# Kernel tuning notes

Measured on AMD Instinct MI355X. Metric: run time of the kernel, lower is better.

The kernel has to match this reference:

```python
import jax, jax.numpy as jnp
import numpy as np

C = 256
CQK = C // 8  # query/key channels


def setup_inputs() -> dict:
    key = jax.random.key(0)
    ks = jax.random.split(key, 7)
    B, H, W = 4, 64, 64
    x = jax.random.normal(ks[0], (B, C, H, W), dtype=jnp.float32)
    # 1x1 conv weights stored as [out_ch, in_ch] (kernel spatial dims are 1)
    sc = 1.0 / np.sqrt(C)
    Wq = jax.random.uniform(ks[1], (CQK, C), jnp.float32, -sc, sc)
    bq = jax.random.uniform(ks[2], (CQK,), jnp.float32, -sc, sc)
    Wk = jax.random.uniform(ks[3], (CQK, C), jnp.float32, -sc, sc)
    bk = jax.random.uniform(ks[4], (CQK,), jnp.float32, -sc, sc)
    Wv = jax.random.uniform(ks[5], (C, C), jnp.float32, -sc, sc)
    bv = jax.random.uniform(ks[6], (C,), jnp.float32, -sc, sc)
    gamma = jnp.zeros((1,), dtype=jnp.float32)
    return {"x": x, "Wq": Wq, "bq": bq, "Wk": Wk, "bk": bk, "Wv": Wv, "bv": bv, "gamma": gamma}


def reference(x, Wq, bq, Wk, bk, Wv, bv, gamma):
    B, Ch, H, W = x.shape
    N = H * W
    xf = x.reshape(B, Ch, N)  # [B, C, N]
    # 1x1 convs == per-pixel linear projections
    q = jnp.einsum('oc,bcn->bno', Wq, xf) + bq  # [B, N, CQK]
    k = jnp.einsum('oc,bcn->bon', Wk, xf) + bk[None, :, None]  # [B, CQK, N]
    v = jnp.einsum('oc,bcn->bon', Wv, xf) + bv[None, :, None]  # [B, C, N]
    s = jnp.einsum('bnd,bdm->bnm', q, k)  # [B, N, N]
    attn = jax.nn.softmax(s, axis=-1)
    # out[b,c,i] = sum_j v[b,c,j] * attn[b,i,j]
    out = jnp.einsum('bcj,bij->bci', v, attn).reshape(B, Ch, H, W)
    return x + gamma[0] * out
```

## Files before the change

kernel.cpp:

```cpp
#include <hip/hip_runtime.h>
#include <math.h>

#define BATCH 4
#define CCH   256
#define DQK   32
#define NPIX  4096
#define LOG2E 1.44269504088896340736f

typedef __attribute__((ext_vector_type(8)))  short          short8_t;
typedef __attribute__((ext_vector_type(4)))  unsigned short ushort4_t;
typedef __attribute__((ext_vector_type(8)))  unsigned short ushort8_t;
typedef __attribute__((ext_vector_type(16))) float          f32x16;
typedef __attribute__((ext_vector_type(2)))  unsigned int   uint2_t;

#if __has_builtin(__builtin_amdgcn_exp2f)
#define EXP2F(x) __builtin_amdgcn_exp2f(x)
#else
#define EXP2F(x) exp2f(x)
#endif

#define MFMA32(a, b, c) __builtin_amdgcn_mfma_f32_32x32x16_bf16(a, b, c, 0, 0, 0)

static __device__ __forceinline__ unsigned short f2bf(float f) {
    union { float f; unsigned int u; } v; v.f = f;
    unsigned int r = v.u + 0x7FFFu + ((v.u >> 16) & 1u);
    return (unsigned short)(r >> 16);
}

static __device__ __forceinline__ short8_t cat8(ushort4_t a, ushort4_t b) {
    ushort8_t c = __builtin_shufflevector(a, b, 0, 1, 2, 3, 4, 5, 6, 7);
    short8_t r; __builtin_memcpy(&r, &c, 16); return r;
}

static __device__ __forceinline__ short8_t u4_to_s8(const unsigned int* u) {
    short8_t r; __builtin_memcpy(&r, u, 16); return r;
}

static __device__ __forceinline__ uint2_t plswap(unsigned int a, unsigned int b) {
#if __has_builtin(__builtin_amdgcn_permlane32_swap)
    return __builtin_amdgcn_permlane32_swap(a, b, false, false);
#else
    const unsigned int sa = (unsigned int)__shfl_xor((int)a, 32);
    const unsigned int sb = (unsigned int)__shfl_xor((int)b, 32);
    const int h = (threadIdx.x >> 5) & 1;
    uint2_t r;
    r.x = h ? sb : a;
    r.y = h ? b : sa;
    return r;
#endif
}

static __device__ __forceinline__ void make_bfrag(
    const f32x16& s, float& l0, float& l1, unsigned int bfr[2][4])
{
    float pv[16];
    #pragma unroll
    for (int r = 0; r < 16; ++r) pv[r] = EXP2F(s[r]);
    #pragma unroll
    for (int r = 0; r < 16; r += 2) { l0 += pv[r]; l1 += pv[r + 1]; }
    unsigned int P[8];
    #pragma unroll
    for (int v = 0; v < 8; ++v)
        P[v] = __builtin_amdgcn_perm(__float_as_uint(pv[2 * v + 1]),
                                     __float_as_uint(pv[2 * v]), 0x07060302u);
    #pragma unroll
    for (int kp = 0; kp < 2; ++kp) {
        const uint2_t r02 = plswap(P[4 * kp + 0], P[4 * kp + 2]);
        const uint2_t r13 = plswap(P[4 * kp + 1], P[4 * kp + 3]);
        bfr[kp][0] = r02.x; bfr[kp][1] = r13.x;
        bfr[kp][2] = r02.y; bfr[kp][3] = r13.y;
    }
}

__global__ __launch_bounds__(256) void wconv_kernel(
    const float* __restrict__ Wq, const float* __restrict__ Wk,
    const float* __restrict__ Wv, unsigned short* __restrict__ wbf)
{
    const int idx = blockIdx.x * 256 + threadIdx.x;
    const int o = idx >> 8, c = idx & 255;
    float v;
    if (o < 32)      v = Wq[o * 256 + c] * LOG2E;
    else if (o < 64) v = Wk[(o - 32) * 256 + c];
    else             v = Wv[(o - 64) * 256 + c];
    wbf[((c >> 3) * 320 + o) * 8 + (c & 7)] = f2bf(v);
}

__global__ __launch_bounds__(256) void xt_kernel(
    const float* __restrict__ x, unsigned short* __restrict__ xfrag)
{
    const int b  = blockIdx.x >> 6;
    const int cg = (blockIdx.x >> 4) & 3;
    const int ng = blockIdx.x & 15;
    const int t  = threadIdx.x;
    const int w = t >> 6, l = t & 63;

    #pragma unroll
    for (int sgl = 0; sgl < 2; ++sgl) {
        const int sg = w * 2 + sgl;
        float f[4][8];
        #pragma unroll
        for (int p = 0; p < 8; ++p) {
            const float* row = x + ((size_t)(b * CCH + cg * 64 + sg * 8 + p)) * NPIX
                                 + ng * 256;
            #pragma unroll
            for (int j = 0; j < 4; ++j)
                f[j][p] = row[j * 64 + l];
        }
        #pragma unroll
        for (int j = 0; j < 4; ++j) {
            unsigned int d[4];
            #pragma unroll
            for (int k = 0; k < 4; ++k)
                d[k] = __builtin_amdgcn_perm(__float_as_uint(f[j][2 * k + 1]),
                                             __float_as_uint(f[j][2 * k]), 0x07060302u);
            const int nt = ng * 8 + j * 2 + (l >> 5);
            unsigned short* dst = xfrag +
                ((((size_t)(b * 128 + nt) * 32) + cg * 8 + sg) * 32 + (l & 31)) * 8;
            *(short8_t*)dst = u4_to_s8(d);
        }
    }
}

__global__ __launch_bounds__(320) void proj_kernel(
    const unsigned short* __restrict__ xfrag, const unsigned short* __restrict__ wbf,
    const float* __restrict__ bq, const float* __restrict__ bk,
    const float* __restrict__ bv,
    unsigned short* __restrict__ qfrag, unsigned short* __restrict__ kfrag,
    unsigned short* __restrict__ vfrag)
{
    __shared__ unsigned short qkb[2 * 2 * 32 * 40];
    __shared__ unsigned short vbuf[4 * 64 * 72];

    const int b   = blockIdx.x >> 6;
    const int nt0 = (blockIdx.x & 63) << 1;
    const int t   = threadIdx.x;
    const int w = t >> 6, lane = t & 63, il = lane & 31, h = lane >> 5;

    float4 bA[4], bB[4];
    #pragma unroll
    for (int g = 0; g < 4; ++g) {
        if (w == 0) {
            bA[g] = *(const float4*)&bq[8 * g + 4 * h];
            bB[g] = *(const float4*)&bk[8 * g + 4 * h];
        } else {
            bA[g] = *(const float4*)&bv[(w - 1) * 64 + 8 * g + 4 * h];
            bB[g] = *(const float4*)&bv[(w - 1) * 64 + 32 + 8 * g + 4 * h];
        }
    }

    f32x16 acc[2][2];
    #pragma unroll
    for (int a = 0; a < 2; ++a)
        #pragma unroll
        for (int i = 0; i < 2; ++i)
            #pragma unroll
            for (int r = 0; r < 16; ++r) acc[a][i][r] = 0.f;

    const unsigned short* wp = wbf + ((size_t)(h * 320 + w * 64 + il)) * 8;
    const unsigned short* xp0 = xfrag + (((size_t)(b * 128 + nt0) * 32 + h) * 32 + il) * 8;
    const unsigned short* xp1 = xp0 + (size_t)32 * 32 * 8;

    #pragma unroll 4
    for (int ks = 0; ks < 16; ++ks) {
        const short8_t af0 = *(const short8_t*)(wp + ks * 5120);
        const short8_t af1 = *(const short8_t*)(wp + ks * 5120 + 256);
        const short8_t bf0 = *(const short8_t*)(xp0 + (size_t)ks * 2 * 256);
        const short8_t bf1 = *(const short8_t*)(xp1 + (size_t)ks * 2 * 256);
        acc[0][0] = MFMA32(af0, bf0, acc[0][0]);
        acc[0][1] = MFMA32(af0, bf1, acc[0][1]);
        acc[1][0] = MFMA32(af1, bf0, acc[1][0]);
        acc[1][1] = MFMA32(af1, bf1, acc[1][1]);
    }

    if (w == 0) {
        #pragma unroll
        for (int it = 0; it < 2; ++it)
            #pragma unroll
            for (int r = 0; r < 16; ++r) {
                const int d = (r & 3) + 8 * (r >> 2) + 4 * h;
                qkb[(it * 2 + 0) * 1280 + il * 40 + d] =
                    f2bf(acc[0][it][r] + bA[r >> 2][r & 3] * LOG2E);
                qkb[(it * 2 + 1) * 1280 + il * 40 + d] =
                    f2bf(acc[1][it][r] + bB[r >> 2][r & 3]);
            }
        #pragma unroll
        for (int it = 0; it < 2; ++it)
            #pragma unroll
            for (int rep = 0; rep < 2; ++rep) {
                const int u = rep * 64 + lane;
                const int slot = u >> 5, n = u & 31;
                ushort4_t qlo = *(const ushort4_t*)&qkb[(it * 2) * 1280 + n * 40 + slot * 8];
                ushort4_t qhi = *(const ushort4_t*)&qkb[(it * 2) * 1280 + n * 40 + slot * 8 + 4];
                ushort4_t klo = *(const ushort4_t*)&qkb[(it * 2 + 1) * 1280 + n * 40 + slot * 8];
                ushort4_t khi = *(const ushort4_t*)&qkb[(it * 2 + 1) * 1280 + n * 40 + slot * 8 + 4];
                const size_t o8 = (((size_t)(b * 128 + nt0 + it) * 4 + slot) * 32 + n) * 8;
                *(short8_t*)(qfrag + o8) = cat8(qlo, qhi);
                *(short8_t*)(kfrag + o8) = cat8(klo, khi);
            }
    } else {
        unsigned short* vb = vbuf + (w - 1) * 64 * 72;
        #pragma unroll
        for (int it = 0; it < 2; ++it)
            #pragma unroll
            for (int r = 0; r < 16; ++r) {
                const int orow = (r & 3) + 8 * (r >> 2) + 4 * h;
                vb[(orow)      * 72 + it * 32 + il] = f2bf(acc[0][it][r] + bA[r >> 2][r & 3]);
                vb[(orow + 32) * 72 + it * 32 + il] = f2bf(acc[1][it][r] + bB[r >> 2][r & 3]);
            }
        #pragma unroll
        for (int rep = 0; rep < 8; ++rep) {
            const int u = rep * 64 + lane;
            const int c = u & 63, m = u >> 6;
            const int it = m >> 2, slot = m & 3;
            ushort4_t lo = *(const ushort4_t*)&vb[c * 72 + it * 32 + slot * 8];
            ushort4_t hi = *(const ushort4_t*)&vb[c * 72 + it * 32 + slot * 8 + 4];
            const size_t o8 = (((size_t)(b * 128 + nt0 + it) * 4 + slot) * 256 +
                               (w - 1) * 64 + c) * 8;
            *(short8_t*)(vfrag + o8) = cat8(lo, hi);
        }
    }
}

struct Stage { short8_t k0, k1, v00, v01, v10, v11; };

__global__ __launch_bounds__(512) void attn_kernel(
    const unsigned short* __restrict__ qfrag,
    const unsigned short* __restrict__ kfrag,
    const unsigned short* __restrict__ vfrag,
    const float* __restrict__ x,
    const float* __restrict__ gamma,
    float* __restrict__ out)
{
    __shared__ float comb[8][64][17];

    const int m8 = blockIdx.x & 7;
    const int b  = m8 >> 1;
    const int itile = ((blockIdx.x >> 3) << 1) | (m8 & 1);
    const int i0 = itile << 6;
    const int t  = threadIdx.x;
    const int w = t >> 6, lane = t & 63, il = lane & 31, h = lane >> 5;
    const int ci = w & 3, jj = w >> 2;
    const int cbase = ci * 64;

    short8_t qf[2][2];
    #pragma unroll
    for (int it = 0; it < 2; ++it)
        #pragma unroll
        for (int ks = 0; ks < 2; ++ks)
            qf[it][ks] = *(const short8_t*)(qfrag +
                (((size_t)(b * 128 + itile * 2 + it) * 4 + ks * 2 + h) * 32 + il) * 8);

    const size_t kbase = (size_t)(b * 128 + jj * 64) * 1024 + h * 256 + il * 8;
    const size_t vbase = (size_t)(b * 128 + jj * 64) * 8192 + h * 2048 + (cbase + il) * 8;

    f32x16 zf;
    #pragma unroll
    for (int r = 0; r < 16; ++r) zf[r] = 0.f;
    f32x16 acc[2][2];
    #pragma unroll
    for (int a = 0; a < 2; ++a)
        #pragma unroll
        for (int c2 = 0; c2 < 2; ++c2) acc[a][c2] = zf;
    float ls[2][2] = {{0.f, 0.f}, {0.f, 0.f}};

    Stage A, B;
    auto load = [&](Stage& S, int jt) {
        const unsigned short* kp = kfrag + kbase + (size_t)jt * 1024;
        S.k0  = *(const short8_t*)kp;
        S.k1  = *(const short8_t*)(kp + 512);
        const unsigned short* vp = vfrag + vbase + (size_t)jt * 8192;
        S.v00 = *(const short8_t*)vp;
        S.v01 = *(const short8_t*)(vp + 4096);
        S.v10 = *(const short8_t*)(vp + 256);
        S.v11 = *(const short8_t*)(vp + 4352);
    };
    auto compute = [&](const Stage& S) {
        f32x16 s0 = MFMA32(S.k0, qf[0][0], zf);
        s0 = MFMA32(S.k1, qf[0][1], s0);
        f32x16 s1 = MFMA32(S.k0, qf[1][0], zf);
        s1 = MFMA32(S.k1, qf[1][1], s1);
        unsigned int bf0[2][4], bf1[2][4];
        make_bfrag(s0, ls[0][0], ls[0][1], bf0);
        make_bfrag(s1, ls[1][0], ls[1][1], bf1);
        acc[0][0] = MFMA32(S.v00, u4_to_s8(bf0[0]), acc[0][0]);
        acc[0][0] = MFMA32(S.v01, u4_to_s8(bf0[1]), acc[0][0]);
        acc[0][1] = MFMA32(S.v10, u4_to_s8(bf0[0]), acc[0][1]);
        acc[0][1] = MFMA32(S.v11, u4_to_s8(bf0[1]), acc[0][1]);
        acc[1][0] = MFMA32(S.v00, u4_to_s8(bf1[0]), acc[1][0]);
        acc[1][0] = MFMA32(S.v01, u4_to_s8(bf1[1]), acc[1][0]);
        acc[1][1] = MFMA32(S.v10, u4_to_s8(bf1[0]), acc[1][1]);
        acc[1][1] = MFMA32(S.v11, u4_to_s8(bf1[1]), acc[1][1]);
    };

    load(A, 0);
    load(B, 1);
    for (int jt = 0; jt < 64; jt += 2) {
        compute(A);
        if (jt + 2 < 64) load(A, jt + 2);
        compute(B);
        if (jt + 3 < 64) load(B, jt + 3);
    }

    float l[2];
    #pragma unroll
    for (int it = 0; it < 2; ++it) {
        l[it] = ls[it][0] + ls[it][1];
        l[it] += __shfl_xor(l[it], 32);
    }
    const float gam = gamma[0];

    #pragma unroll
    for (int it = 0; it < 2; ++it) {
        __syncthreads();
        #pragma unroll
        for (int r = 0; r < 16; ++r)
            comb[w][lane][r] = jj ? acc[it][0][r] : acc[it][1][r];
        comb[w][lane][16] = l[it];
        __syncthreads();
        const int pw = w ^ 4;
        const float lt = l[it] + comb[pw][lane][16];
        const float sc = gam / lt;
        #pragma unroll
        for (int r = 0; r < 16; ++r) {
            const float o = (jj ? acc[it][1][r] : acc[it][0][r]) + comb[pw][lane][r];
            const int c = cbase + jj * 32 + (r & 3) + 8 * (r >> 2) + 4 * h;
            const size_t idx = ((size_t)(b * CCH + c)) * NPIX + i0 + it * 32 + il;
            out[idx] = x[idx] + o * sc;
        }
    }
}

extern "C" void kernel_launch(void* const* d_in, const int* in_sizes, int n_in,
                              void* d_out, int out_size, void* d_ws, size_t ws_size,
                              hipStream_t stream) {
    const float* x     = (const float*)d_in[0];
    const float* Wq    = (const float*)d_in[1];
    const float* bq    = (const float*)d_in[2];
    const float* Wk    = (const float*)d_in[3];
    const float* bk    = (const float*)d_in[4];
    const float* Wv    = (const float*)d_in[5];
    const float* bv    = (const float*)d_in[6];
    const float* gamma = (const float*)d_in[7];
    float* out = (float*)d_out;

    unsigned short* ws    = (unsigned short*)d_ws;
    unsigned short* wbf   = ws;
    unsigned short* xfrag = ws + 81920;
    unsigned short* qfrag = xfrag + (size_t)4194304;
    unsigned short* kfrag = qfrag + (size_t)524288;
    unsigned short* vfrag = kfrag + (size_t)524288;

    wconv_kernel<<<dim3(320), dim3(256), 0, stream>>>(Wq, Wk, Wv, wbf);
    xt_kernel<<<dim3(256), dim3(256), 0, stream>>>(x, xfrag);
    proj_kernel<<<dim3(256), dim3(320), 0, stream>>>(
        xfrag, wbf, bq, bk, bv, qfrag, kfrag, vfrag);
    attn_kernel<<<dim3(256), dim3(512), 0, stream>>>(
        qfrag, kfrag, vfrag, x, gamma, out);
}
```

Baseline: 154.6 us.

## Repartition attention waves into 2 channel x 4 key splits with wider V tiles

Changes the per-block work split from 4 channel groups x 2 key halves to 2 channel groups of 128 x 4 key quarters. Each wave now holds 8 accumulator tiles and processes 32 key tiles instead of 64. K fragments stay double-buffered while V is loaded once per step and reused across both query tiles. Fewer channel groups per wave means each QK^T score tile and its softmax conversion are computed by fewer waves, so the intent is to cut redundant QK and exp work. The cost is higher register pressure and a final cross-wave reduction that now needs four LDS rounds per query tile with more barriers.

```diff
diff --git a/kernel.cpp b/kernel.cpp
--- a/kernel.cpp
+++ b/kernel.cpp
@@ -221,7 +221,7 @@
     }
 }
 
-struct Stage { short8_t k0, k1, v00, v01, v10, v11; };
+struct KStage { short8_t k0, k1; };
 
 __global__ __launch_bounds__(512) void attn_kernel(
     const unsigned short* __restrict__ qfrag,
@@ -239,8 +239,7 @@
     const int i0 = itile << 6;
     const int t  = threadIdx.x;
     const int w = t >> 6, lane = t & 63, il = lane & 31, h = lane >> 5;
-    const int ci = w & 3, jj = w >> 2;
-    const int cbase = ci * 64;
+    const int ci = w & 1, jj = w >> 1;
 
     short8_t qf[2][2];
     #pragma unroll
@@ -250,55 +249,66 @@
             qf[it][ks] = *(const short8_t*)(qfrag +
                 (((size_t)(b * 128 + itile * 2 + it) * 4 + ks * 2 + h) * 32 + il) * 8);
 
-    const size_t kbase = (size_t)(b * 128 + jj * 64) * 1024 + h * 256 + il * 8;
-    const size_t vbase = (size_t)(b * 128 + jj * 64) * 8192 + h * 2048 + (cbase + il) * 8;
+    const size_t kbase = (size_t)(b * 128 + jj * 32) * 1024 + h * 256 + il * 8;
+    const size_t vbase = (size_t)(b * 128 + jj * 32) * 8192 + h * 2048 +
+                         (ci * 128 + il) * 8;
 
     f32x16 zf;
     #pragma unroll
     for (int r = 0; r < 16; ++r) zf[r] = 0.f;
-    f32x16 acc[2][2];
+    f32x16 acc[2][4];
     #pragma unroll
     for (int a = 0; a < 2; ++a)
         #pragma unroll
-        for (int c2 = 0; c2 < 2; ++c2) acc[a][c2] = zf;
+        for (int c4 = 0; c4 < 4; ++c4) acc[a][c4] = zf;
     float ls[2][2] = {{0.f, 0.f}, {0.f, 0.f}};
 
-    Stage A, B;
-    auto load = [&](Stage& S, int jt) {
+    KStage A, B;
+    short8_t v[4][2];
+
+    auto loadK = [&](KStage& S, int jt) {
         const unsigned short* kp = kfrag + kbase + (size_t)jt * 1024;
-        S.k0  = *(const short8_t*)kp;
-        S.k1  = *(const short8_t*)(kp + 512);
+        S.k0 = *(const short8_t*)kp;
+        S.k1 = *(const short8_t*)(kp + 512);
+    };
+    auto loadV = [&](int jt) {
         const unsigned short* vp = vfrag + vbase + (size_t)jt * 8192;
-        S.v00 = *(const short8_t*)vp;
-        S.v01 = *(const short8_t*)(vp + 4096);
-        S.v10 = *(const short8_t*)(vp + 256);
-        S.v11 = *(const short8_t*)(vp + 4352);
+        #pragma unroll
+        for (int ct = 0; ct < 4; ++ct) {
+            v[ct][0] = *(const short8_t*)(vp + ct * 256);
+            v[ct][1] = *(const short8_t*)(vp + ct * 256 + 4096);
+        }
     };
-    auto compute = [&](const Stage& S) {
-        f32x16 s0 = MFMA32(S.k0, qf[0][0], zf);
-        s0 = MFMA32(S.k1, qf[0][1], s0);
-        f32x16 s1 = MFMA32(S.k0, qf[1][0], zf);
-        s1 = MFMA32(S.k1, qf[1][1], s1);
-        unsigned int bf0[2][4], bf1[2][4];
-        make_bfrag(s0, ls[0][0], ls[0][1], bf0);
-        make_bfrag(s1, ls[1][0], ls[1][1], bf1);
-        acc[0][0] = MFMA32(S.v00, u4_to_s8(bf0[0]), acc[0][0]);
-        acc[0][0] = MFMA32(S.v01, u4_to_s8(bf0[1]), acc[0][0]);
-        acc[0][1] = MFMA32(S.v10, u4_to_s8(bf0[0]), acc[0][1]);
-        acc[0][1] = MFMA32(S.v11, u4_to_s8(bf0[1]), acc[0][1]);
-        acc[1][0] = MFMA32(S.v00, u4_to_s8(bf1[0]), acc[1][0]);
-        acc[1][0] = MFMA32(S.v01, u4_to_s8(bf1[1]), acc[1][0]);
-        acc[1][1] = MFMA32(S.v10, u4_to_s8(bf1[0]), acc[1][1]);
-        acc[1][1] = MFMA32(S.v11, u4_to_s8(bf1[1]), acc[1][1]);
+    auto step = [&](KStage& S, int kNext) {
+        f32x16 s = MFMA32(S.k0, qf[0][0], zf);
+        s = MFMA32(S.k1, qf[0][1], s);
+        unsigned int bfr[2][4];
+        make_bfrag(s, ls[0][0], ls[0][1], bfr);
+        #pragma unroll
+        for (int ct = 0; ct < 4; ++ct) {
+            acc[0][ct] = MFMA32(v[ct][0], u4_to_s8(bfr[0]), acc[0][ct]);
+            acc[0][ct] = MFMA32(v[ct][1], u4_to_s8(bfr[1]), acc[0][ct]);
+        }
+        s = MFMA32(S.k0, qf[1][0], zf);
+        s = MFMA32(S.k1, qf[1][1], s);
+        if (kNext < 32) loadK(S, kNext);
+        make_bfrag(s, ls[1][0], ls[1][1], bfr);
+        #pragma unroll
+        for (int ct = 0; ct < 4; ++ct) {
+            acc[1][ct] = MFMA32(v[ct][0], u4_to_s8(bfr[0]), acc[1][ct]);
+            acc[1][ct] = MFMA32(v[ct][1], u4_to_s8(bfr[1]), acc[1][ct]);
+        }
     };
 
-    load(A, 0);
-    load(B, 1);
-    for (int jt = 0; jt < 64; jt += 2) {
-        compute(A);
-        if (jt + 2 < 64) load(A, jt + 2);
-        compute(B);
-        if (jt + 3 < 64) load(B, jt + 3);
+    loadK(A, 0);
+    loadK(B, 1);
+    loadV(0);
+    #pragma unroll 1
+    for (int jt = 0; jt < 32; jt += 2) {
+        step(A, jt + 2);
+        loadV(jt + 1);
+        step(B, jt + 3);
+        if (jt + 2 < 32) loadV(jt + 2);
     }
 
     float l[2];
@@ -308,24 +318,35 @@
         l[it] += __shfl_xor(l[it], 32);
     }
     const float gam = gamma[0];
+    const int p1 = ci + 2 * ((jj + 1) & 3);
+    const int p2 = ci + 2 * ((jj + 2) & 3);
+    const int p3 = ci + 2 * ((jj + 3) & 3);
+    float lt[2];
 
     #pragma unroll
     for (int it = 0; it < 2; ++it) {
-        __syncthreads();
-        #pragma unroll
-        for (int r = 0; r < 16; ++r)
-            comb[w][lane][r] = jj ? acc[it][0][r] : acc[it][1][r];
-        comb[w][lane][16] = l[it];
-        __syncthreads();
-        const int pw = w ^ 4;
-        const float lt = l[it] + comb[pw][lane][16];
-        const float sc = gam / lt;
-        #pragma unroll
-        for (int r = 0; r < 16; ++r) {
-            const float o = (jj ? acc[it][1][r] : acc[it][0][r]) + comb[pw][lane][r];
-            const int c = cbase + jj * 32 + (r & 3) + 8 * (r >> 2) + 4 * h;
-            const size_t idx = ((size_t)(b * CCH + c)) * NPIX + i0 + it * 32 + il;
-            out[idx] = x[idx] + o * sc;
+        #pragma unroll 1
+        for (int ct = 0; ct < 4; ++ct) {
+            __syncthreads();
+            #pragma unroll
+            for (int r = 0; r < 16; ++r) comb[w][lane][r] = acc[it][ct][r];
+            if (ct == 0) comb[w][lane][16] = l[it];
+            __syncthreads();
+            if (ct == 0)
+                lt[it] = l[it] + comb[p1][lane][16] + comb[p2][lane][16] +
+                         comb[p3][lane][16];
+            if (jj == ct) {
+                const float sc = gam / lt[it];
+                #pragma unroll
+                for (int r = 0; r < 16; ++r) {
+                    const float o = acc[it][ct][r] + comb[p1][lane][r] +
+                                    comb[p2][lane][r] + comb[p3][lane][r];
+                    const int c = ci * 128 + ct * 32 + (r & 3) + 8 * (r >> 2) + 4 * h;
+                    const size_t idx = ((size_t)(b * CCH + c)) * NPIX + i0 +
+                                       it * 32 + il;
+                    out[idx] = x[idx] + o * sc;
+                }
+            }
         }
     }
 }
```

Measured after the change: 170.0 us. 10.0% more time.
